# Kernel tuning notes

Measured on AMD Instinct MI355X. Metric: run time of the kernel, lower is better.

## Reference

```python
import jax, jax.numpy as jnp
import numpy as np

N = 100000   # nodes
E = 1600000  # edges
IN = 128     # in_feats
H = 64       # h_feats
NEG_SLOPE = 0.2  # DGL GATConv default negative_slope


def setup_inputs() -> dict:
    key = jax.random.key(0)
    ks = jax.random.split(key, 6)
    in_feat = jax.random.normal(ks[0], (N, IN), jnp.float32)
    src = jax.random.randint(ks[1], (E,), 0, N)
    dst = jax.random.randint(ks[2], (E,), 0, N)

    def mk(k, din, dout):
        k1, k2, k3 = jax.random.split(k, 3)
        W = jax.random.normal(k1, (dout, din), jnp.float32) * np.float32(1.0 / np.sqrt(din))
        al = jax.random.normal(k2, (dout,), jnp.float32) * 0.1
        ar = jax.random.normal(k3, (dout,), jnp.float32) * 0.1
        b = jnp.zeros((dout,), jnp.float32)
        return W, al, ar, b

    W1, al1, ar1, b1 = mk(ks[3], IN, H)
    W2, al2, ar2, b2 = mk(ks[4], H, H)
    W3, al3, ar3, b3 = mk(ks[5], H, H)
    return dict(in_feat=in_feat, W1=W1, al1=al1, ar1=ar1, b1=b1,
                W2=W2, al2=al2, ar2=ar2, b2=b2,
                W3=W3, al3=al3, ar3=ar3, b3=b3,
                src=src, dst=dst)


def gat_layer(x, W, al, ar, b, src, dst):
    # DGL GATConv, num_heads=1: project, edge attention, segment softmax over dst, scatter-agg, bias, ReLU
    feat = x @ W.T                                   # [N, H]
    el = feat @ al                                   # [N] a_l . Wh_i
    er = feat @ ar                                   # [N] a_r . Wh_j
    e = jax.nn.leaky_relu(el[src] + er[dst], NEG_SLOPE)   # [E]
    m = jax.ops.segment_max(e, dst, num_segments=N)       # per-dst max (stable softmax)
    ee = jnp.exp(e - m[dst])                               # [E]
    denom = jax.ops.segment_sum(ee, dst, num_segments=N)  # [N]
    alpha = ee / denom[dst]                                # [E]
    out = jax.ops.segment_sum(feat[src] * alpha[:, None], dst, num_segments=N)  # [N, H]
    return jax.nn.relu(out + b)


def reference(in_feat, W1, al1, ar1, b1, W2, al2, ar2, b2, W3, al3, ar3, b3, src, dst):
    h = gat_layer(in_feat, W1, al1, ar1, b1, src, dst)
    h = gat_layer(h, W2, al2, ar2, b2, src, dst)
    h = gat_layer(h, W3, al3, ar3, b3, src, dst)
    return h
```

## Files before the change

### kernel.cpp

```cpp
#include <hip/hip_runtime.h>
#include <math.h>

#define NNODES 100000
#define NEDGES 1600000
#define HF 64
#define NBUCK_SHIFT 9
#define NBUCK 256
#define NBUCK_USED ((NNODES + 511) >> 9)
#define KC_BLOCKS 512
#define KB_BLOCKS 1024

__global__ __launch_bounds__(256) void k_bcount(
    const int* __restrict__ dst, int* __restrict__ bcnt, int E)
{
    __shared__ int hist[NBUCK];
    const int tid = threadIdx.x;
    const int EPB = (E + KC_BLOCKS - 1) / KC_BLOCKS;
    const int e0 = blockIdx.x * EPB;
    const int e1 = min(E, e0 + EPB);
    hist[tid] = 0;
    __syncthreads();
    for (int i = e0 + tid; i < e1; i += 256)
        atomicAdd(&hist[dst[i] >> NBUCK_SHIFT], 1);
    __syncthreads();
    if (hist[tid]) atomicAdd(&bcnt[tid], hist[tid]);
}

__global__ __launch_bounds__(256) void k_bscan(
    const int* __restrict__ bcnt, int* __restrict__ gcur, int* __restrict__ bstart)
{
    __shared__ int s[256];
    const int tid = threadIdx.x;
    int own = bcnt[tid];
    s[tid] = own;
    __syncthreads();
    for (int off = 1; off < 256; off <<= 1) {
        int t = (tid >= off) ? s[tid - off] : 0;
        __syncthreads();
        s[tid] += t;
        __syncthreads();
    }
    int excl = s[tid] - own;
    gcur[tid] = excl;
    bstart[tid] = excl;
    if (tid == 255) bstart[256] = s[255];
}

__global__ __launch_bounds__(256) void k_bucket(
    const int* __restrict__ src, const int* __restrict__ dst,
    int* __restrict__ gcur, int2* __restrict__ ebuf2, int E)
{
    __shared__ int hist[NBUCK];
    const int tid = threadIdx.x;
    const int EPB = (E + KB_BLOCKS - 1) / KB_BLOCKS;
    const int e0 = blockIdx.x * EPB;
    const int e1 = min(E, e0 + EPB);

    hist[tid] = 0;
    __syncthreads();
    for (int i = e0 + tid; i < e1; i += 256)
        atomicAdd(&hist[dst[i] >> NBUCK_SHIFT], 1);
    __syncthreads();
    int cnt = hist[tid];
    int base = (cnt > 0) ? atomicAdd(&gcur[tid], cnt) : 0;
    __syncthreads();
    hist[tid] = base;
    __syncthreads();
    for (int i = e0 + tid; i < e1; i += 256) {
        int d = dst[i];
        int r = atomicAdd(&hist[d >> NBUCK_SHIFT], 1);
        ebuf2[r] = make_int2(src[i], d);
    }
}

__global__ __launch_bounds__(256) void k_local(
    const int2* __restrict__ ebuf2, const int* __restrict__ bstart,
    int* __restrict__ deg, int* __restrict__ cur, int* __restrict__ esrc)
{
    __shared__ int lhist[512];
    __shared__ int lcur[512];
    __shared__ int s[256];
    const int b = blockIdx.x;
    const int tid = threadIdx.x;
    const int e0 = bstart[b];
    const int e1 = bstart[b + 1];
    const int n0 = b << NBUCK_SHIFT;

    lhist[tid] = 0;
    lhist[tid + 256] = 0;
    __syncthreads();
    for (int i = e0 + tid; i < e1; i += 256)
        atomicAdd(&lhist[ebuf2[i].y - n0], 1);
    __syncthreads();

    int v0 = lhist[2 * tid], v1 = lhist[2 * tid + 1];
    int tsum = v0 + v1;
    s[tid] = tsum;
    __syncthreads();
    for (int off = 1; off < 256; off <<= 1) {
        int t = (tid >= off) ? s[tid - off] : 0;
        __syncthreads();
        s[tid] += t;
        __syncthreads();
    }
    int run = s[tid] - tsum;
    lcur[2 * tid] = run;
    lcur[2 * tid + 1] = run + v0;
    int node0 = n0 + 2 * tid;
    if (node0 < NNODES)     { deg[node0] = v0;     cur[node0] = e0 + run + v0; }
    if (node0 + 1 < NNODES) { deg[node0 + 1] = v1; cur[node0 + 1] = e0 + run + v0 + v1; }
    __syncthreads();

    for (int i = e0 + tid; i < e1; i += 256) {
        int2 e = ebuf2[i];
        int p = atomicAdd(&lcur[e.y - n0], 1);
        esrc[e0 + p] = e.x;
    }
}

template <int K>
__global__ __launch_bounds__(256) void gemm_tile(
    const float* __restrict__ x, const float* __restrict__ W,
    const float* __restrict__ al, const float* __restrict__ ar,
    float* __restrict__ feat, float* __restrict__ el, float* __restrict__ er,
    int n)
{
    constexpr int KS = 32;
    __shared__ float xs[KS][132];
    __shared__ float wt[KS][68];

    const int tid = threadIdx.x;
    const int tx = tid & 15;
    const int ty = tid >> 4;
    const int row0 = blockIdx.x * 128;

    float acc[8][4];
#pragma unroll
    for (int i = 0; i < 8; ++i)
#pragma unroll
        for (int j = 0; j < 4; ++j) acc[i][j] = 0.f;

    for (int ks = 0; ks < K; ks += KS) {
        if (ks) __syncthreads();
#pragma unroll
        for (int jj = 0; jj < 4; ++jj) {
            int j = tid + jj * 256;
            int r = j >> 3;
            int k4 = j & 7;
            int gr = row0 + r;
            float4 v = make_float4(0.f, 0.f, 0.f, 0.f);
            if (gr < n) v = *(const float4*)(x + (size_t)gr * K + ks + 4 * k4);
            xs[4 * k4 + 0][r] = v.x;
            xs[4 * k4 + 1][r] = v.y;
            xs[4 * k4 + 2][r] = v.z;
            xs[4 * k4 + 3][r] = v.w;
        }
#pragma unroll
        for (int jj = 0; jj < 2; ++jj) {
            int j = tid + jj * 256;
            int c = j >> 3;
            int k4 = j & 7;
            float4 v = *(const float4*)(W + (size_t)c * K + ks + 4 * k4);
            wt[4 * k4 + 0][c] = v.x;
            wt[4 * k4 + 1][c] = v.y;
            wt[4 * k4 + 2][c] = v.z;
            wt[4 * k4 + 3][c] = v.w;
        }
        __syncthreads();

#pragma unroll 8
        for (int k = 0; k < KS; ++k) {
            float4 a0 = *(const float4*)&xs[k][8 * ty + 0];
            float4 a1 = *(const float4*)&xs[k][8 * ty + 4];
            float4 b  = *(const float4*)&wt[k][4 * tx];
            float ar_[8] = {a0.x, a0.y, a0.z, a0.w, a1.x, a1.y, a1.z, a1.w};
            float bc[4] = {b.x, b.y, b.z, b.w};
#pragma unroll
            for (int i = 0; i < 8; ++i)
#pragma unroll
                for (int j = 0; j < 4; ++j)
                    acc[i][j] += ar_[i] * bc[j];
        }
    }

    const float4 ald = *(const float4*)(al + 4 * tx);
    const float4 ard = *(const float4*)(ar + 4 * tx);
#pragma unroll
    for (int i = 0; i < 8; ++i) {
        int row = row0 + 8 * ty + i;
        float pl = acc[i][0] * ald.x + acc[i][1] * ald.y +
                   acc[i][2] * ald.z + acc[i][3] * ald.w;
        float pr = acc[i][0] * ard.x + acc[i][1] * ard.y +
                   acc[i][2] * ard.z + acc[i][3] * ard.w;
#pragma unroll
        for (int off = 8; off >= 1; off >>= 1) {
            pl += __shfl_xor(pl, off);
            pr += __shfl_xor(pr, off);
        }
        if (row < n) {
            float4 st = make_float4(acc[i][0], acc[i][1], acc[i][2], acc[i][3]);
            *(float4*)(feat + (size_t)row * HF + 4 * tx) = st;
            if (tx == 0) { el[row] = pl; er[row] = pr; }
        }
    }
}

__global__ __launch_bounds__(256) void node_agg(
    const int* __restrict__ cur, const int* __restrict__ deg,
    const int* __restrict__ esrc,
    const float* __restrict__ el, const float* __restrict__ er,
    const float* __restrict__ feat, const float* __restrict__ bias,
    float* __restrict__ out, int n)
{
    const int node = blockIdx.x * 4 + (threadIdx.x >> 6);
    if (node >= n) return;
    const int lane = threadIdx.x & 63;
    const int cx = lane & 15;
    const int lg = lane >> 4;

    const int dg = deg[node];

    if (dg == 0) {
        if (lane < 16) {
            float4 b4 = *(const float4*)(bias + 4 * cx);
            float4 o;
            o.x = fmaxf(b4.x, 0.f); o.y = fmaxf(b4.y, 0.f);
            o.z = fmaxf(b4.z, 0.f); o.w = fmaxf(b4.w, 0.f);
            *(float4*)(out + (size_t)node * HF + 4 * cx) = o;
        }
        return;
    }

    const int base = cur[node] - dg;
    const float erd = er[node];

    if (dg <= 32) {
        int sreg = 0;
        if (lane < dg) sreg = esrc[base + lane];
        float elv = 0.f;
        if (lane < dg) elv = el[sreg];

        int sj[8];
#pragma unroll
        for (int t = 0; t < 8; ++t) sj[t] = __shfl(sreg, lg + 4 * t);

        float4 f[8];
#pragma unroll
        for (int t = 0; t < 8; ++t)
            if (lg + 4 * t < dg)
                f[t] = *(const float4*)(feat + (size_t)sj[t] * HF + 4 * cx);

        float ereg = -INFINITY;
        if (lane < dg) {
            float e = elv + erd;
            ereg = (e >= 0.f) ? e : 0.2f * e;
        }
        float m = ereg;
#pragma unroll
        for (int off = 32; off >= 1; off >>= 1)
            m = fmaxf(m, __shfl_xor(m, off));
        float ee = __expf(ereg - m);
        float den = ee;
#pragma unroll
        for (int off = 32; off >= 1; off >>= 1)
            den += __shfl_xor(den, off);

        float4 c[4];
#pragma unroll
        for (int q = 0; q < 4; ++q) c[q] = make_float4(0.f, 0.f, 0.f, 0.f);
#pragma unroll
        for (int t = 0; t < 8; ++t) {
            float w = __shfl(ee, lg + 4 * t);
            if (lg + 4 * t < dg) {
                c[t & 3].x += w * f[t].x;
                c[t & 3].y += w * f[t].y;
                c[t & 3].z += w * f[t].z;
                c[t & 3].w += w * f[t].w;
            }
        }
        float4 acc;
        acc.x = (c[0].x + c[1].x) + (c[2].x + c[3].x);
        acc.y = (c[0].y + c[1].y) + (c[2].y + c[3].y);
        acc.z = (c[0].z + c[1].z) + (c[2].z + c[3].z);
        acc.w = (c[0].w + c[1].w) + (c[2].w + c[3].w);
#pragma unroll
        for (int off = 16; off <= 32; off <<= 1) {
            acc.x += __shfl_xor(acc.x, off);
            acc.y += __shfl_xor(acc.y, off);
            acc.z += __shfl_xor(acc.z, off);
            acc.w += __shfl_xor(acc.w, off);
        }
        if (lane < 16) {
            float inv = 1.f / den;
            float4 b4 = *(const float4*)(bias + 4 * cx);
            float4 o;
            o.x = fmaxf(acc.x * inv + b4.x, 0.f);
            o.y = fmaxf(acc.y * inv + b4.y, 0.f);
            o.z = fmaxf(acc.z * inv + b4.z, 0.f);
            o.w = fmaxf(acc.w * inv + b4.w, 0.f);
            *(float4*)(out + (size_t)node * HF + 4 * cx) = o;
        }
        return;
    }

    if (dg <= 64) {
        int sreg = 0;
        float ereg = -INFINITY;
        if (lane < dg) {
            sreg = esrc[base + lane];
            float e = el[sreg] + erd;
            ereg = (e >= 0.f) ? e : 0.2f * e;
        }
        float m = ereg;
#pragma unroll
        for (int off = 32; off >= 1; off >>= 1)
            m = fmaxf(m, __shfl_xor(m, off));
        float ee = __expf(ereg - m);
        float den = ee;
#pragma unroll
        for (int off = 32; off >= 1; off >>= 1)
            den += __shfl_xor(den, off);

        float4 c[4];
#pragma unroll
        for (int q = 0; q < 4; ++q) c[q] = make_float4(0.f, 0.f, 0.f, 0.f);
        for (int j0 = 0; j0 < dg; j0 += 16) {
#pragma unroll
            for (int q = 0; q < 4; ++q) {
                int jj = j0 + lg + 4 * q;
                int   s = __shfl(sreg, jj & 63);
                float w = __shfl(ee, jj & 63);
                if (jj < dg) {
                    float4 fv = *(const float4*)(feat + (size_t)s * HF + 4 * cx);
                    c[q].x += w * fv.x;
                    c[q].y += w * fv.y;
                    c[q].z += w * fv.z;
                    c[q].w += w * fv.w;
                }
            }
        }
        float4 acc;
        acc.x = (c[0].x + c[1].x) + (c[2].x + c[3].x);
        acc.y = (c[0].y + c[1].y) + (c[2].y + c[3].y);
        acc.z = (c[0].z + c[1].z) + (c[2].z + c[3].z);
        acc.w = (c[0].w + c[1].w) + (c[2].w + c[3].w);
#pragma unroll
        for (int off = 16; off <= 32; off <<= 1) {
            acc.x += __shfl_xor(acc.x, off);
            acc.y += __shfl_xor(acc.y, off);
            acc.z += __shfl_xor(acc.z, off);
            acc.w += __shfl_xor(acc.w, off);
        }
        if (lane < 16) {
            float inv = 1.f / den;
            float4 b4 = *(const float4*)(bias + 4 * cx);
            float4 o;
            o.x = fmaxf(acc.x * inv + b4.x, 0.f);
            o.y = fmaxf(acc.y * inv + b4.y, 0.f);
            o.z = fmaxf(acc.z * inv + b4.z, 0.f);
            o.w = fmaxf(acc.w * inv + b4.w, 0.f);
            *(float4*)(out + (size_t)node * HF + 4 * cx) = o;
        }
        return;
    }

    float m = -INFINITY;
    for (int j = lane; j < dg; j += 64) {
        int s = esrc[base + j];
        float e = el[s] + erd;
        e = (e >= 0.f) ? e : 0.2f * e;
        m = fmaxf(m, e);
    }
#pragma unroll
    for (int off = 32; off >= 1; off >>= 1)
        m = fmaxf(m, __shfl_xor(m, off));

    float acc = 0.f, den = 0.f;
    for (int j = 0; j < dg; ++j) {
        int s = esrc[base + j];
        float e = el[s] + erd;
        e = (e >= 0.f) ? e : 0.2f * e;
        float ee = __expf(e - m);
        den += ee;
        acc += ee * feat[(size_t)s * HF + lane];
    }
    out[(size_t)node * HF + lane] = fmaxf(acc / den + bias[lane], 0.f);
}

extern "C" void kernel_launch(void* const* d_in, const int* in_sizes, int n_in,
                              void* d_out, int out_size, void* d_ws, size_t ws_size,
                              hipStream_t stream) {
    const int N = NNODES;
    const int E = NEDGES;

    const float* in_feat = (const float*)d_in[0];
    const float* W1 = (const float*)d_in[1];
    const float* al1 = (const float*)d_in[2];
    const float* ar1 = (const float*)d_in[3];
    const float* b1 = (const float*)d_in[4];
    const float* W2 = (const float*)d_in[5];
    const float* al2 = (const float*)d_in[6];
    const float* ar2 = (const float*)d_in[7];
    const float* b2 = (const float*)d_in[8];
    const float* W3 = (const float*)d_in[9];
    const float* al3 = (const float*)d_in[10];
    const float* ar3 = (const float*)d_in[11];
    const float* b3 = (const float*)d_in[12];
    const int* src = (const int*)d_in[13];
    const int* dst = (const int*)d_in[14];

    float* ws = (float*)d_ws;
    float* feat = ws;
    float* h1   = feat + (size_t)N * HF;
    float* h2   = h1 + (size_t)N * HF;
    float* el   = h2 + (size_t)N * HF;
    float* er   = el + N;
    int* deg    = (int*)(er + N);
    int* cur    = deg + N;
    int* bcnt   = cur + N;
    int* bstart = bcnt + 256;
    int* gcur   = bstart + 260;
    int* esrc   = gcur + 256;
    int2* ebuf2 = (int2*)h1;

    const int gEdge = (E + 255) / 256;
    const int gNode4 = (N + 3) / 4;
    const int gTile = (N + 127) / 128;
    (void)gEdge;

    hipMemsetAsync(bcnt, 0, NBUCK * 4, stream);
    k_bcount<<<KC_BLOCKS, 256, 0, stream>>>(dst, bcnt, E);
    k_bscan<<<1, 256, 0, stream>>>(bcnt, gcur, bstart);
    k_bucket<<<KB_BLOCKS, 256, 0, stream>>>(src, dst, gcur, ebuf2, E);
    k_local<<<NBUCK_USED, 256, 0, stream>>>(ebuf2, bstart, deg, cur, esrc);

    float* out = (float*)d_out;

    gemm_tile<128><<<gTile, 256, 0, stream>>>(in_feat, W1, al1, ar1, feat, el, er, N);
    node_agg<<<gNode4, 256, 0, stream>>>(cur, deg, esrc, el, er, feat, b1, h1, N);

    gemm_tile<64><<<gTile, 256, 0, stream>>>(h1, W2, al2, ar2, feat, el, er, N);
    node_agg<<<gNode4, 256, 0, stream>>>(cur, deg, esrc, el, er, feat, b2, h2, N);

    gemm_tile<64><<<gTile, 256, 0, stream>>>(h2, W3, al3, ar3, feat, el, er, N);
    node_agg<<<gNode4, 256, 0, stream>>>(cur, deg, esrc, el, er, feat, b3, out, N);
}
```

Before: 343.0 us.

## Pack bucketed edges into one int and prefetch GEMM tiles through registers

The bucketing pass now stores each edge as a single 32-bit word (src shifted left by 9, OR'd with the dst offset inside its 512-node bucket) instead of an int2. This halves the intermediate edge buffer traffic in k_bucket and k_local. The projection GEMM now uses a 64-wide K chunk and register-prefetches the next chunk's x/W tiles while computing the current one. That raises register and LDS use, which may reduce occupancy. The packing only works while src stays below 2^23.

```diff
diff --git a/kernel.cpp b/kernel.cpp
--- a/kernel.cpp
+++ b/kernel.cpp
@@ -48,7 +48,7 @@
 
 __global__ __launch_bounds__(256) void k_bucket(
     const int* __restrict__ src, const int* __restrict__ dst,
-    int* __restrict__ gcur, int2* __restrict__ ebuf2, int E)
+    int* __restrict__ gcur, int* __restrict__ epack, int E)
 {
     __shared__ int hist[NBUCK];
     const int tid = threadIdx.x;
@@ -69,12 +69,12 @@
     for (int i = e0 + tid; i < e1; i += 256) {
         int d = dst[i];
         int r = atomicAdd(&hist[d >> NBUCK_SHIFT], 1);
-        ebuf2[r] = make_int2(src[i], d);
+        epack[r] = (src[i] << NBUCK_SHIFT) | (d & 511);
     }
 }
 
 __global__ __launch_bounds__(256) void k_local(
-    const int2* __restrict__ ebuf2, const int* __restrict__ bstart,
+    const int* __restrict__ epack, const int* __restrict__ bstart,
     int* __restrict__ deg, int* __restrict__ cur, int* __restrict__ esrc)
 {
     __shared__ int lhist[512];
@@ -90,7 +90,7 @@
     lhist[tid + 256] = 0;
     __syncthreads();
     for (int i = e0 + tid; i < e1; i += 256)
-        atomicAdd(&lhist[ebuf2[i].y - n0], 1);
+        atomicAdd(&lhist[epack[i] & 511], 1);
     __syncthreads();
 
     int v0 = lhist[2 * tid], v1 = lhist[2 * tid + 1];
@@ -112,9 +112,9 @@
     __syncthreads();
 
     for (int i = e0 + tid; i < e1; i += 256) {
-        int2 e = ebuf2[i];
-        int p = atomicAdd(&lcur[e.y - n0], 1);
-        esrc[e0 + p] = e.x;
+        int p = epack[i];
+        int pos = atomicAdd(&lcur[p & 511], 1);
+        esrc[e0 + pos] = ((unsigned)p) >> NBUCK_SHIFT;
     }
 }
 
@@ -125,7 +125,8 @@
     float* __restrict__ feat, float* __restrict__ el, float* __restrict__ er,
     int n)
 {
-    constexpr int KS = 32;
+    constexpr int KS = 64;
+    constexpr int NC = K / KS;
     __shared__ float xs[KS][132];
     __shared__ float wt[KS][68];
 
@@ -140,34 +141,59 @@
 #pragma unroll
         for (int j = 0; j < 4; ++j) acc[i][j] = 0.f;
 
-    for (int ks = 0; ks < K; ks += KS) {
-        if (ks) __syncthreads();
-#pragma unroll
-        for (int jj = 0; jj < 4; ++jj) {
-            int j = tid + jj * 256;
-            int r = j >> 3;
-            int k4 = j & 7;
-            int gr = row0 + r;
-            float4 v = make_float4(0.f, 0.f, 0.f, 0.f);
-            if (gr < n) v = *(const float4*)(x + (size_t)gr * K + ks + 4 * k4);
-            xs[4 * k4 + 0][r] = v.x;
-            xs[4 * k4 + 1][r] = v.y;
-            xs[4 * k4 + 2][r] = v.z;
-            xs[4 * k4 + 3][r] = v.w;
-        }
-#pragma unroll
-        for (int jj = 0; jj < 2; ++jj) {
-            int j = tid + jj * 256;
-            int c = j >> 3;
-            int k4 = j & 7;
-            float4 v = *(const float4*)(W + (size_t)c * K + ks + 4 * k4);
-            wt[4 * k4 + 0][c] = v.x;
-            wt[4 * k4 + 1][c] = v.y;
-            wt[4 * k4 + 2][c] = v.z;
-            wt[4 * k4 + 3][c] = v.w;
-        }
-        __syncthreads();
-
+    float4 xr[8], wr[4];
+
+#pragma unroll
+    for (int jj = 0; jj < 8; ++jj) {
+        int j = tid + jj * 256;
+        int gr = row0 + (j >> 4);
+        int k4 = j & 15;
+        xr[jj] = make_float4(0.f, 0.f, 0.f, 0.f);
+        if (gr < n) xr[jj] = *(const float4*)(x + (size_t)gr * K + 4 * k4);
+    }
+#pragma unroll
+    for (int jj = 0; jj < 4; ++jj) {
+        int j = tid + jj * 256;
+        wr[jj] = *(const float4*)(W + (size_t)(j >> 4) * K + 4 * (j & 15));
+    }
+#pragma unroll
+    for (int jj = 0; jj < 8; ++jj) {
+        int j = tid + jj * 256;
+        int r = j >> 4, k4 = j & 15;
+        xs[4 * k4 + 0][r] = xr[jj].x;
+        xs[4 * k4 + 1][r] = xr[jj].y;
+        xs[4 * k4 + 2][r] = xr[jj].z;
+        xs[4 * k4 + 3][r] = xr[jj].w;
+    }
+#pragma unroll
+    for (int jj = 0; jj < 4; ++jj) {
+        int j = tid + jj * 256;
+        int c = j >> 4, k4 = j & 15;
+        wt[4 * k4 + 0][c] = wr[jj].x;
+        wt[4 * k4 + 1][c] = wr[jj].y;
+        wt[4 * k4 + 2][c] = wr[jj].z;
+        wt[4 * k4 + 3][c] = wr[jj].w;
+    }
+    __syncthreads();
+
+#pragma unroll
+    for (int c = 0; c < NC; ++c) {
+        if (c + 1 < NC) {
+            const int ks = (c + 1) * KS;
+#pragma unroll
+            for (int jj = 0; jj < 8; ++jj) {
+                int j = tid + jj * 256;
+                int gr = row0 + (j >> 4);
+                int k4 = j & 15;
+                xr[jj] = make_float4(0.f, 0.f, 0.f, 0.f);
+                if (gr < n) xr[jj] = *(const float4*)(x + (size_t)gr * K + ks + 4 * k4);
+            }
+#pragma unroll
+            for (int jj = 0; jj < 4; ++jj) {
+                int j = tid + jj * 256;
+                wr[jj] = *(const float4*)(W + (size_t)(j >> 4) * K + ks + 4 * (j & 15));
+            }
+        }
 #pragma unroll 8
         for (int k = 0; k < KS; ++k) {
             float4 a0 = *(const float4*)&xs[k][8 * ty + 0];
@@ -180,6 +206,28 @@
 #pragma unroll
                 for (int j = 0; j < 4; ++j)
                     acc[i][j] += ar_[i] * bc[j];
+        }
+        if (c + 1 < NC) {
+            __syncthreads();
+#pragma unroll
+            for (int jj = 0; jj < 8; ++jj) {
+                int j = tid + jj * 256;
+                int r = j >> 4, k4 = j & 15;
+                xs[4 * k4 + 0][r] = xr[jj].x;
+                xs[4 * k4 + 1][r] = xr[jj].y;
+                xs[4 * k4 + 2][r] = xr[jj].z;
+                xs[4 * k4 + 3][r] = xr[jj].w;
+            }
+#pragma unroll
+            for (int jj = 0; jj < 4; ++jj) {
+                int j = tid + jj * 256;
+                int cc = j >> 4, k4 = j & 15;
+                wt[4 * k4 + 0][cc] = wr[jj].x;
+                wt[4 * k4 + 1][cc] = wr[jj].y;
+                wt[4 * k4 + 2][cc] = wr[jj].z;
+                wt[4 * k4 + 3][cc] = wr[jj].w;
+            }
+            __syncthreads();
         }
     }
 
@@ -421,18 +469,16 @@
     int* bstart = bcnt + 256;
     int* gcur   = bstart + 260;
     int* esrc   = gcur + 256;
-    int2* ebuf2 = (int2*)h1;
-
-    const int gEdge = (E + 255) / 256;
+    int* epack  = (int*)h1;
+
     const int gNode4 = (N + 3) / 4;
     const int gTile = (N + 127) / 128;
-    (void)gEdge;
 
     hipMemsetAsync(bcnt, 0, NBUCK * 4, stream);
     k_bcount<<<KC_BLOCKS, 256, 0, stream>>>(dst, bcnt, E);
     k_bscan<<<1, 256, 0, stream>>>(bcnt, gcur, bstart);
-    k_bucket<<<KB_BLOCKS, 256, 0, stream>>>(src, dst, gcur, ebuf2, E);
-    k_local<<<NBUCK_USED, 256, 0, stream>>>(ebuf2, bstart, deg, cur, esrc);
+    k_bucket<<<KB_BLOCKS, 256, 0, stream>>>(src, dst, gcur, epack, E);
+    k_local<<<NBUCK_USED, 256, 0, stream>>>(epack, bstart, deg, cur, esrc);
 
     float* out = (float*)d_out;
 
```

After: 355.0 us. 1.03x slower.
